# Performance work log

Hardware: AMD Instinct MI355X
Metric: run time of the kernel (lower is better)

Reference implementation:

```python
import jax, jax.numpy as jnp
import numpy as np

B, S, HID = 2, 2048, 2048
H, D = 16, 128
K = 4  # conv kernel size
EPS_L2 = 1e-6
EPS_RMS = 1e-5


def _l2norm(x, eps=EPS_L2):
  return x * jax.lax.rsqrt(jnp.sum(x * x, axis=-1, keepdims=True) + eps)


def _causal_dwconv_silu(x, w):
  # x: [B,S,C], w: [K,1,C] depthwise causal conv, then SiLU
  y = jax.lax.conv_general_dilated(
      x, w, window_strides=(1,), padding=[(w.shape[0] - 1, 0)],
      dimension_numbers=('NWC', 'WIO', 'NWC'), feature_group_count=x.shape[-1])
  return jax.nn.silu(y)


def _delta_rule(q, k, v, g, beta, scale):
  # q,k,v,g: [B,S,H,D]; beta: [B,S,H]
  qs = (q * scale).transpose(1, 0, 2, 3)  # time-major [S,B,H,D]
  ks = k.transpose(1, 0, 2, 3)
  vs = v.transpose(1, 0, 2, 3)
  gs = g.transpose(1, 0, 2, 3)
  bs = beta.transpose(1, 0, 2)  # [S,B,H]

  def step(Sst, inp):
    qt, kt, vt, gt, bt = inp  # [B,H,D], bt [B,H]
    Sst = Sst * jnp.exp(gt)[..., :, None]              # decay on k-dim: [B,H,Dk,Dv]
    err = vt - jnp.einsum('bhk,bhkv->bhv', kt, Sst)    # delta error [B,H,Dv]
    Sst = Sst + bt[..., None, None] * kt[..., :, None] * err[..., None, :]
    ot = jnp.einsum('bhk,bhkv->bhv', qt, Sst)
    return Sst, ot

  S0 = jnp.zeros((q.shape[0], q.shape[2], q.shape[3], v.shape[3]), q.dtype)
  _, outs = jax.lax.scan(step, S0, (qs, ks, vs, gs, bs))
  return outs.transpose(1, 0, 2, 3)  # [B,S,H,Dv]


def setup_inputs() -> dict:
  key = jax.random.key(0)
  ks = jax.random.split(key, 20)
  sh = 1.0 / np.sqrt(HID)
  sd = 1.0 / np.sqrt(D)
  inp = {
      'hidden_states': jax.random.normal(ks[0], (B, S, HID), jnp.float32),
      'Wq': jax.random.normal(ks[1], (HID, H * D), jnp.float32) * sh,
      'Wk': jax.random.normal(ks[2], (HID, H * D), jnp.float32) * sh,
      'Wv': jax.random.normal(ks[3], (HID, H * D), jnp.float32) * sh,
      'conv_q': jax.random.normal(ks[4], (K, 1, H * D), jnp.float32) * 0.5,
      'conv_k': jax.random.normal(ks[5], (K, 1, H * D), jnp.float32) * 0.5,
      'conv_v': jax.random.normal(ks[6], (K, 1, H * D), jnp.float32) * 0.5,
      'Wb': jax.random.normal(ks[7], (HID, H), jnp.float32) * sh,
      'Wfa': jax.random.normal(ks[8], (HID, D), jnp.float32) * sh,
      'Wfb': jax.random.normal(ks[9], (D, H * D), jnp.float32) * sd,
      'Wga': jax.random.normal(ks[10], (HID, D), jnp.float32) * sh,
      'Wgb': jax.random.normal(ks[11], (D, H * D), jnp.float32) * sd,
      'A_log': jnp.log(jax.random.uniform(ks[12], (1, 1, H, 1), jnp.float32, 1e-9, 16.0)),
      'dt_bias': jnp.ones((H * D,), jnp.float32),
      'rms_scale': jnp.ones((D,), jnp.float32),
      'Wo': jax.random.normal(ks[13], (H * D, HID), jnp.float32) * sd,
  }
  return inp


def reference(hidden_states, Wq, Wk, Wv, conv_q, conv_k, conv_v, Wb, Wfa, Wfb,
              Wga, Wgb, A_log, dt_bias, rms_scale, Wo):
  b, s, _ = hidden_states.shape
  q = _l2norm(jnp.einsum('bsd,de->bse', hidden_states, Wq).reshape(b, s, H, D))
  k = _l2norm(jnp.einsum('bsd,de->bse', hidden_states, Wk).reshape(b, s, H, D))
  v = jnp.einsum('bsd,de->bse', hidden_states, Wv).reshape(b, s, H, D)

  q = _causal_dwconv_silu(q.reshape(b, s, -1), conv_q).reshape(b, s, H, D)
  k = _causal_dwconv_silu(k.reshape(b, s, -1), conv_k).reshape(b, s, H, D)
  v = _causal_dwconv_silu(v.reshape(b, s, -1), conv_v).reshape(b, s, H, D)

  beta = jax.nn.sigmoid(jnp.einsum('bsd,dh->bsh', hidden_states, Wb))  # [B,S,H]

  # fused KDA forget gate (log-space, per k-channel)
  g_lin = jnp.einsum('bse,ef->bsf', jnp.einsum('bsd,de->bse', hidden_states, Wfa), Wfb)
  sp = jax.nn.softplus(g_lin + dt_bias).reshape(b, s, H, D)
  g_forget = -jnp.exp(A_log) * sp  # [B,S,H,D]

  attn = _delta_rule(q, k, v, g_forget, beta, scale=D ** -0.5)  # [B,S,H,D]

  # fused RMSNorm + sigmoid gate over head_dim
  gate = jnp.einsum('bse,ef->bsf', jnp.einsum('bsd,de->bse', hidden_states, Wga), Wgb).reshape(b, s, H, D)
  normed = attn * jax.lax.rsqrt(jnp.mean(attn * attn, axis=-1, keepdims=True) + EPS_RMS) * rms_scale
  out = (normed * jax.nn.sigmoid(gate)).reshape(b, s, -1)
  return jnp.einsum('bse,ed->bsd', out, Wo)
```

## Files before the change

kernel.cpp:

```cpp
#include <hip/hip_runtime.h>
#include <cstdint>

#define BB 2
#define SS 2048
#define HID_ 2048
#define HH 16
#define DD 128
#define HD 2048
#define MM 4096
#define CC 64
#define NCH 32
#define NU 1024

typedef unsigned short u16;
typedef __bf16 bf16x8 __attribute__((ext_vector_type(8)));
typedef float f32x4 __attribute__((ext_vector_type(4)));
typedef unsigned short u16x8 __attribute__((ext_vector_type(8)));

__device__ __forceinline__ u16 f2bf(float f) {
  unsigned u = __float_as_uint(f);
  u += 0x7FFFu + ((u >> 16) & 1u);
  return (u16)(u >> 16);
}
__device__ __forceinline__ float blo(unsigned u) { return __uint_as_float(u << 16); }
__device__ __forceinline__ float bhi(unsigned u) { return __uint_as_float(u & 0xffff0000u); }
__device__ __forceinline__ float sigmoidf_(float x) { return 1.0f / (1.0f + __expf(-x)); }

__device__ __forceinline__ void gll16(const void* g, void* l) {
  __builtin_amdgcn_global_load_lds((const __attribute__((address_space(1))) void*)g,
                                   (__attribute__((address_space(3))) void*)l, 16, 0, 0);
}

__global__ void cvt_bf16_kernel(const float* __restrict__ in, u16* __restrict__ out, int n) {
  int i = blockIdx.x * blockDim.x + threadIdx.x;
  if (i < n) out[i] = f2bf(in[i]);
}

__global__ __launch_bounds__(256) void transpose_bf16_kernel(
    const float* __restrict__ in, u16* __restrict__ out, int K, int N) {
  __shared__ float tile[32][33];
  int n0 = blockIdx.x * 32, k0 = blockIdx.y * 32;
  int tx = threadIdx.x, ty = threadIdx.y;
#pragma unroll
  for (int i = 0; i < 32; i += 8)
    tile[ty + i][tx] = in[(size_t)(k0 + ty + i) * N + (n0 + tx)];
  __syncthreads();
#pragma unroll
  for (int i = 0; i < 32; i += 8)
    out[(size_t)(n0 + ty + i) * K + (k0 + tx)] = f2bf(tile[tx][ty + i]);
}

__global__ __launch_bounds__(256) void gemm_bf16_kernel(
    const u16* __restrict__ A, const u16* __restrict__ Bt, float* __restrict__ C,
    int M, int N, int K) {
  __shared__ u16 As[128 * 32];
  __shared__ u16 Bs[128 * 32];
  const int tid = threadIdx.x;
  const int tileN = blockIdx.x * 128, tileM = blockIdx.y * 128;
  const int lane = tid & 63, wv = tid >> 6;
  const int wm = (wv & 1) * 64, wn = (wv >> 1) * 64;
  const int frm = lane & 15, fk = (lane >> 4) * 8;
  const int srow0 = 32 * wv + (lane >> 2);
  const int scol8 = (lane & 3) * 8;
  const u16* Ab0 = A + (size_t)(tileM + srow0) * K + scol8;
  const u16* Ab1 = A + (size_t)(tileM + srow0 + 16) * K + scol8;
  const u16* Bb0 = Bt + (size_t)(tileN + srow0) * K + scol8;
  const u16* Bb1 = Bt + (size_t)(tileN + srow0 + 16) * K + scol8;
  u16* AsL0 = &As[1024 * wv];
  u16* AsL1 = &As[1024 * wv + 512];
  u16* BsL0 = &Bs[1024 * wv];
  u16* BsL1 = &Bs[1024 * wv + 512];
  f32x4 acc[4][4];
#pragma unroll
  for (int i = 0; i < 4; ++i)
#pragma unroll
    for (int j = 0; j < 4; ++j) acc[i][j] = (f32x4)0.0f;
  for (int k0 = 0; k0 < K; k0 += 32) {
    gll16(Ab0 + k0, AsL0);
    gll16(Ab1 + k0, AsL1);
    gll16(Bb0 + k0, BsL0);
    gll16(Bb1 + k0, BsL1);
    __syncthreads();
    bf16x8 af[4], bfr[4];
#pragma unroll
    for (int t = 0; t < 4; ++t)
      af[t] = *(const bf16x8*)(&As[(wm + t * 16 + frm) * 32 + fk]);
#pragma unroll
    for (int t = 0; t < 4; ++t)
      bfr[t] = *(const bf16x8*)(&Bs[(wn + t * 16 + frm) * 32 + fk]);
#pragma unroll
    for (int mt = 0; mt < 4; ++mt)
#pragma unroll
      for (int nt = 0; nt < 4; ++nt)
        acc[mt][nt] = __builtin_amdgcn_mfma_f32_16x16x32_bf16(af[mt], bfr[nt], acc[mt][nt], 0, 0, 0);
    __syncthreads();
  }
  const int crow = (lane >> 4) * 4, ccol = lane & 15;
#pragma unroll
  for (int mt = 0; mt < 4; ++mt)
#pragma unroll
    for (int nt = 0; nt < 4; ++nt) {
      float* cp = C + (size_t)(tileM + wm + mt * 16 + crow) * N + (tileN + wn + nt * 16 + ccol);
#pragma unroll
      for (int i = 0; i < 4; ++i) cp[(size_t)i * N] = acc[mt][nt][i];
    }
}

__global__ __launch_bounds__(256) void l2norm_kernel(float* __restrict__ x) {
  int idx = blockIdx.x * 4 + (threadIdx.x >> 6);
  int lane = threadIdx.x & 63;
  float* p = x + (size_t)idx * DD;
  float2 v = *(float2*)(p + lane * 2);
  float ss = v.x * v.x + v.y * v.y;
#pragma unroll
  for (int o = 32; o > 0; o >>= 1) ss += __shfl_xor(ss, o);
  float r = rsqrtf(ss + 1e-6f);
  v.x *= r; v.y *= r;
  *(float2*)(p + lane * 2) = v;
}

__global__ void conv_silu_kernel(const float* __restrict__ x, const float* __restrict__ w,
                                 float* __restrict__ y, int n) {
  int id = blockIdx.x * blockDim.x + threadIdx.x;
  if (id >= n) return;
  int c = id & (HD - 1);
  int s = (id >> 11) & (SS - 1);
  float acc = 0.f;
#pragma unroll
  for (int t = 0; t < 4; ++t) {
    int sp = s - 3 + t;
    if (sp >= 0) acc += w[t * HD + c] * x[id + (t - 3) * HD];
  }
  y[id] = acc * sigmoidf_(acc);
}

__global__ __launch_bounds__(256) void beta_kernel(const float* __restrict__ hid,
                                                   const float* __restrict__ Wb,
                                                   float* __restrict__ beta) {
  int row = blockIdx.x;
  int tid = threadIdx.x;
  int h = tid & 15, chunk = tid >> 4;
  const float* hp = hid + (size_t)row * HID_;
  float acc = 0.f;
  int d0 = chunk * 128;
  for (int i = 0; i < 128; ++i) acc += hp[d0 + i] * Wb[(size_t)(d0 + i) * 16 + h];
  __shared__ float red[256];
  red[tid] = acc;
  __syncthreads();
  if (tid < 16) {
    float s = 0.f;
#pragma unroll
    for (int j = 0; j < 16; ++j) s += red[j * 16 + tid];
    beta[(size_t)row * 16 + tid] = 1.f / (1.f + __expf(-s));
  }
}

__global__ void kda_g_kernel(float* __restrict__ glin, const float* __restrict__ A_log,
                             const float* __restrict__ dt_bias, int n) {
  int id = blockIdx.x * blockDim.x + threadIdx.x;
  if (id >= n) return;
  int c = id & (HD - 1);
  int h = c >> 7;
  float x = glin[id] + dt_bias[c];
  float sp = (x > 20.f) ? x : log1pf(__expf(x));
  glin[id] = -__expf(A_log[h]) * sp;
}

__global__ __launch_bounds__(256) void chunk_prep(
    const float* __restrict__ q, const float* __restrict__ k, float* __restrict__ v,
    const float* __restrict__ g, const float* __restrict__ beta,
    u16* __restrict__ P, u16* __restrict__ Gt, float* __restrict__ dl,
    u16* __restrict__ Qp, u16* __restrict__ Xp) {
  __shared__ float gcl[CC * DD];
  __shared__ u16 kb[CC * DD];
  __shared__ u16 Ml[CC * CC];
  __shared__ float betal[CC];
  const int tid = threadIdx.x;
  const int chunk = blockIdx.x & 31, bh = blockIdx.x >> 5;
  const int h = bh & 15, b = bh >> 4;
  const size_t unit = (size_t)bh * NCH + chunk;
  const size_t base = ((size_t)b * SS + (size_t)chunk * CC) * HD + (size_t)h * DD;
  const float scale = 0.08838834764831845f;

  {
    int t = tid >> 2, seg = tid & 3;
    const float* kr = k + base + (size_t)t * HD + seg * 32;
    float kv[32];
#pragma unroll
    for (int i = 0; i < 8; ++i) *(f32x4*)&kv[4 * i] = *(const f32x4*)(kr + 4 * i);
    unsigned pu[16];
#pragma unroll
    for (int i = 0; i < 16; ++i)
      pu[i] = (unsigned)f2bf(kv[2 * i]) | ((unsigned)f2bf(kv[2 * i + 1]) << 16);
    uint4* dst = (uint4*)&kb[t * DD + seg * 32];
#pragma unroll
    for (int i = 0; i < 4; ++i) dst[i] = make_uint4(pu[4 * i], pu[4 * i + 1], pu[4 * i + 2], pu[4 * i + 3]);
  }
  if (tid < CC) betal[tid] = beta[((size_t)b * SS + (size_t)chunk * CC + tid) * HH + h];
  if (tid < DD) {
    int c = tid;
    float acc = 0.f;
    for (int t = 0; t < CC; ++t) {
      acc += g[base + (size_t)t * HD + c];
      gcl[t * DD + c] = acc;
    }
  }
  __syncthreads();

  {
    const int t = tid >> 2, cg = tid & 3, c0 = cg * 32;
    float kt[32], qt[32], gct[32];
#pragma unroll
    for (int i = 0; i < 8; ++i) {
      uint2 kk = ((const uint2*)&kb[t * DD + c0])[i];
      kt[4 * i + 0] = blo(kk.x); kt[4 * i + 1] = bhi(kk.x);
      kt[4 * i + 2] = blo(kk.y); kt[4 * i + 3] = bhi(kk.y);
      *(f32x4*)&gct[4 * i] = *(const f32x4*)&gcl[t * DD + c0 + 4 * i];
      *(f32x4*)&qt[4 * i] = *(const f32x4*)(q + base + (size_t)t * HD + c0 + 4 * i);
    }
#pragma unroll
    for (int i = 0; i < 32; ++i) qt[i] *= scale;
    const float bt = betal[t];
    const int jmax = ((tid >> 6) << 4) + 15;
    for (int j = 0; j <= jmax; ++j) {
      float accA = 0.f, accG = 0.f;
#pragma unroll
      for (int i = 0; i < 8; ++i) {
        uint2 kk = ((const uint2*)&kb[j * DD + c0])[i];
        f32x4 gj = *(const f32x4*)&gcl[j * DD + c0 + 4 * i];
        float e0 = __expf(gct[4 * i + 0] - gj[0]);
        float e1 = __expf(gct[4 * i + 1] - gj[1]);
        float e2 = __expf(gct[4 * i + 2] - gj[2]);
        float e3 = __expf(gct[4 * i + 3] - gj[3]);
        float p0 = blo(kk.x) * e0, p1 = bhi(kk.x) * e1;
        float p2 = blo(kk.y) * e2, p3 = bhi(kk.y) * e3;
        accA += kt[4 * i + 0] * p0 + kt[4 * i + 1] * p1 + kt[4 * i + 2] * p2 + kt[4 * i + 3] * p3;
        accG += qt[4 * i + 0] * p0 + qt[4 * i + 1] * p1 + qt[4 * i + 2] * p2 + qt[4 * i + 3] * p3;
      }
      accA += __shfl_xor(accA, 1); accA += __shfl_xor(accA, 2);
      accG += __shfl_xor(accG, 1); accG += __shfl_xor(accG, 2);
      if (cg == 0) {
        if (j <= t) {
          Gt[unit * 4096 + t * 64 + j] = f2bf(accG);
          if (j < t) Ml[t * CC + j] = f2bf(bt * accA);
        } else {
          Gt[unit * 4096 + t * 64 + j] = 0;
        }
      }
    }
    if (cg == 0)
      for (int j = jmax + 1; j < CC; ++j) Gt[unit * 4096 + t * 64 + j] = 0;
  }
  __syncthreads();

  {
    const int t = tid >> 2, seg = tid & 3;
    const size_t rb = base + (size_t)t * HD + seg * 32;
    const int e0 = t * DD + seg * 32;
    float qv[32];
#pragma unroll
    for (int i = 0; i < 8; ++i) *(f32x4*)&qv[4 * i] = *(const f32x4*)(q + rb + 4 * i);
    unsigned pu[16];
#pragma unroll
    for (int i = 0; i < 16; ++i) {
      float a = qv[2 * i] * scale * __expf(gcl[e0 + 2 * i]);
      float c2 = qv[2 * i + 1] * scale * __expf(gcl[e0 + 2 * i + 1]);
      pu[i] = (unsigned)f2bf(a) | ((unsigned)f2bf(c2) << 16);
    }
    uint4* dst = (uint4*)(Qp + unit * 8192 + t * 128 + seg * 32);
    dst[0] = make_uint4(pu[0], pu[1], pu[2], pu[3]);
    dst[1] = make_uint4(pu[4], pu[5], pu[6], pu[7]);
    ((uint4*)(Qp + unit * 8192 + t * 128 + seg * 32 + 16))[0] = make_uint4(pu[8], pu[9], pu[10], pu[11]);
    ((uint4*)(Qp + unit * 8192 + t * 128 + seg * 32 + 24))[0] = make_uint4(pu[12], pu[13], pu[14], pu[15]);
  }
  {
    const int c = tid >> 1, hf = tid & 1;
    const float glast = gcl[(CC - 1) * DD + c];
    unsigned pu[16];
#pragma unroll
    for (int i = 0; i < 16; ++i) {
      int t0 = hf * 32 + 2 * i;
      float x0 = blo((unsigned)kb[t0 * DD + c]) * __expf(glast - gcl[t0 * DD + c]);
      float x1 = blo((unsigned)kb[(t0 + 1) * DD + c]) * __expf(glast - gcl[(t0 + 1) * DD + c]);
      pu[i] = (unsigned)f2bf(x0) | ((unsigned)f2bf(x1) << 16);
    }
    uint4* dst = (uint4*)(Xp + unit * 8192 + c * 64 + hf * 32);
#pragma unroll
    for (int i = 0; i < 4; ++i)
      dst[i] = make_uint4(pu[4 * i], pu[4 * i + 1], pu[4 * i + 2], pu[4 * i + 3]);
  }
  if (tid < DD) dl[unit * DD + tid] = __expf(gcl[(CC - 1) * DD + tid]);

  {
    const int col = tid, c = col & 127;
    const bool isV = col < 128;
    float X[CC];
#pragma unroll
    for (int t = 0; t < CC; ++t) {
      float rv;
      if (isV) rv = v[base + (size_t)t * HD + c];
      else rv = blo((unsigned)kb[t * DD + c]) * __expf(gcl[t * DD + c]);
      X[t] = betal[t] * rv;
    }
#pragma unroll
    for (int i = 1; i < CC; ++i) {
      float acc = X[i];
#pragma unroll
      for (int jb = 0; jb * 8 < i; ++jb) {
        uint4 mm = *(const uint4*)&Ml[i * CC + jb * 8];
        const int j0 = jb * 8;
        if (j0 + 0 < i) acc -= blo(mm.x) * X[j0 + 0];
        if (j0 + 1 < i) acc -= bhi(mm.x) * X[j0 + 1];
        if (j0 + 2 < i) acc -= blo(mm.y) * X[j0 + 2];
        if (j0 + 3 < i) acc -= bhi(mm.y) * X[j0 + 3];
        if (j0 + 4 < i) acc -= blo(mm.z) * X[j0 + 4];
        if (j0 + 5 < i) acc -= bhi(mm.z) * X[j0 + 5];
        if (j0 + 6 < i) acc -= blo(mm.w) * X[j0 + 6];
        if (j0 + 7 < i) acc -= bhi(mm.w) * X[j0 + 7];
      }
      X[i] = acc;
    }
#pragma unroll
    for (int t = 0; t < CC; ++t) {
      if (isV) v[base + (size_t)t * HD + c] = X[t];
      else P[unit * 8192 + t * DD + c] = f2bf(X[t]);
    }
  }
}

__global__ __launch_bounds__(256) void state_pass(
    const u16* __restrict__ P, const u16* __restrict__ Xp,
    const float* __restrict__ Uvg, const float* __restrict__ dl,
    u16* __restrict__ Sst) {
  __shared__ u16 Pb[64 * 136];
  __shared__ u16 Xb[128 * 72];
  __shared__ float S[128 * 20];
  __shared__ float U[64 * 20];
  __shared__ float dll[128];
  const int tid = threadIdx.x;
  const int vs = blockIdx.x, bh = blockIdx.y;
  const int h = bh & 15, b = bh >> 4;
  for (int i = tid; i < 128 * 20; i += 256) S[i] = 0.f;
  __syncthreads();
  for (int c = 0; c < NCH; ++c) {
    const size_t unit = (size_t)bh * NCH + c;
    const size_t base = ((size_t)b * SS + (size_t)c * CC) * HD + (size_t)h * DD + vs * 16;
#pragma unroll
    for (int r = 0; r < 4; ++r) {
      int e = r * 256 + tid;
      int t = e >> 4, kp = (e & 15) * 8;
      *(uint4*)&Pb[t * 136 + kp] = ((const uint4*)(P + unit * 8192))[e];
      int kk = e >> 3, tp = (e & 7) * 8;
      *(uint4*)&Xb[kk * 72 + tp] = ((const uint4*)(Xp + unit * 8192))[e];
    }
    {
      int t = tid >> 2, cg = tid & 3;
      *(f32x4*)&U[t * 20 + cg * 4] = *(const f32x4*)(Uvg + base + (size_t)t * HD + cg * 4);
    }
    if (tid < 128) dll[tid] = dl[unit * DD + tid];
    {
      int v2 = tid >> 4, kq = tid & 15;
      unsigned pu[4];
#pragma unroll
      for (int j = 0; j < 4; ++j) {
        float a = S[(kq * 8 + 2 * j) * 20 + v2];
        float bb = S[(kq * 8 + 2 * j + 1) * 20 + v2];
        pu[j] = (unsigned)f2bf(a) | ((unsigned)f2bf(bb) << 16);
      }
      *(uint4*)(Sst + unit * 16384 + (size_t)(vs * 16 + v2) * 128 + kq * 8) =
          make_uint4(pu[0], pu[1], pu[2], pu[3]);
    }
    __syncthreads();
    {
      const int t = tid >> 2, cg = tid & 3;
      f32x4 u = *(f32x4*)&U[t * 20 + cg * 4];
      f32x4 acc = (f32x4)0.f;
      for (int kk = 0; kk < 128; kk += 4) {
        uint2 pk = *(const uint2*)&Pb[t * 136 + kk];
        f32x4 s0 = *(const f32x4*)&S[(kk + 0) * 20 + cg * 4];
        f32x4 s1 = *(const f32x4*)&S[(kk + 1) * 20 + cg * 4];
        f32x4 s2 = *(const f32x4*)&S[(kk + 2) * 20 + cg * 4];
        f32x4 s3 = *(const f32x4*)&S[(kk + 3) * 20 + cg * 4];
        acc += blo(pk.x) * s0;
        acc += bhi(pk.x) * s1;
        acc += blo(pk.y) * s2;
        acc += bhi(pk.y) * s3;
      }
      u -= acc;
      *(f32x4*)&U[t * 20 + cg * 4] = u;
    }
    __syncthreads();
    {
      const int kk = tid >> 1, cg2 = tid & 1;
      f32x4 sa = *(f32x4*)&S[kk * 20 + cg2 * 8];
      f32x4 sb = *(f32x4*)&S[kk * 20 + cg2 * 8 + 4];
      float dk = dll[kk];
      sa *= dk; sb *= dk;
      for (int t4 = 0; t4 < 64; t4 += 4) {
        uint2 xv = *(const uint2*)&Xb[kk * 72 + t4];
        float x0 = blo(xv.x), x1 = bhi(xv.x), x2 = blo(xv.y), x3 = bhi(xv.y);
        f32x4 u0a = *(const f32x4*)&U[(t4 + 0) * 20 + cg2 * 8];
        f32x4 u0b = *(const f32x4*)&U[(t4 + 0) * 20 + cg2 * 8 + 4];
        f32x4 u1a = *(const f32x4*)&U[(t4 + 1) * 20 + cg2 * 8];
        f32x4 u1b = *(const f32x4*)&U[(t4 + 1) * 20 + cg2 * 8 + 4];
        f32x4 u2a = *(const f32x4*)&U[(t4 + 2) * 20 + cg2 * 8];
        f32x4 u2b = *(const f32x4*)&U[(t4 + 2) * 20 + cg2 * 8 + 4];
        f32x4 u3a = *(const f32x4*)&U[(t4 + 3) * 20 + cg2 * 8];
        f32x4 u3b = *(const f32x4*)&U[(t4 + 3) * 20 + cg2 * 8 + 4];
        sa += x0 * u0a; sb += x0 * u0b;
        sa += x1 * u1a; sb += x1 * u1b;
        sa += x2 * u2a; sb += x2 * u2b;
        sa += x3 * u3a; sb += x3 * u3b;
      }
      *(f32x4*)&S[kk * 20 + cg2 * 8] = sa;
      *(f32x4*)&S[kk * 20 + cg2 * 8 + 4] = sb;
    }
    __syncthreads();
  }
}

__global__ __launch_bounds__(256) void out_pass(
    const u16* __restrict__ P, const u16* __restrict__ Qp,
    const u16* __restrict__ G, const u16* __restrict__ Sst,
    const float* __restrict__ Uvg, float* __restrict__ attn) {
  __shared__ u16 Sb[128 * 136];
  __shared__ u16 Pb[64 * 136];
  __shared__ u16 Qb[64 * 136];
  __shared__ u16 Gb[64 * 72];
  __shared__ u16 Ub[128 * 72];
  const int tid = threadIdx.x;
  const int unit = blockIdx.x;
  const int bh = unit >> 5, c = unit & 31;
  const int h = bh & 15, b = bh >> 4;
  const size_t base = ((size_t)b * SS + (size_t)c * CC) * HD + (size_t)h * DD;
#pragma unroll
  for (int r = 0; r < 8; ++r) {
    int e = r * 256 + tid;
    int v = e >> 4, kp = (e & 15) * 8;
    *(uint4*)&Sb[v * 136 + kp] = ((const uint4*)(Sst + (size_t)unit * 16384))[e];
  }
#pragma unroll
  for (int r = 0; r < 4; ++r) {
    int e = r * 256 + tid;
    int t = e >> 4, kp = (e & 15) * 8;
    *(uint4*)&Pb[t * 136 + kp] = ((const uint4*)(P + (size_t)unit * 8192))[e];
    *(uint4*)&Qb[t * 136 + kp] = ((const uint4*)(Qp + (size_t)unit * 8192))[e];
  }
#pragma unroll
  for (int r = 0; r < 2; ++r) {
    int e = r * 256 + tid;
    int t = e >> 3, jp = (e & 7) * 8;
    *(uint4*)&Gb[t * 72 + jp] = ((const uint4*)(G + (size_t)unit * 4096))[e];
  }
  __syncthreads();
  const int w = tid >> 6, lane = tid & 63;
  const int frm = lane & 15, fk = (lane >> 4) * 8;
  const int crow = (lane >> 4) * 4, ccol = lane & 15;
  bf16x8 Pf[4], Qf[4], Gf[2];
#pragma unroll
  for (int kb2 = 0; kb2 < 4; ++kb2) {
    Pf[kb2] = *(const bf16x8*)&Pb[(w * 16 + frm) * 136 + kb2 * 32 + fk];
    Qf[kb2] = *(const bf16x8*)&Qb[(w * 16 + frm) * 136 + kb2 * 32 + fk];
  }
#pragma unroll
  for (int kb2 = 0; kb2 < 2; ++kb2)
    Gf[kb2] = *(const bf16x8*)&Gb[(w * 16 + frm) * 72 + kb2 * 32 + fk];
  f32x4 aps[8], ao[8];
#pragma unroll
  for (int nt = 0; nt < 8; ++nt) { aps[nt] = (f32x4)0.f; ao[nt] = (f32x4)0.f; }
#pragma unroll
  for (int nt = 0; nt < 8; ++nt)
#pragma unroll
    for (int kb2 = 0; kb2 < 4; ++kb2) {
      bf16x8 sf = *(const bf16x8*)&Sb[(nt * 16 + frm) * 136 + kb2 * 32 + fk];
      aps[nt] = __builtin_amdgcn_mfma_f32_16x16x32_bf16(Pf[kb2], sf, aps[nt], 0, 0, 0);
      ao[nt] = __builtin_amdgcn_mfma_f32_16x16x32_bf16(Qf[kb2], sf, ao[nt], 0, 0, 0);
    }
#pragma unroll
  for (int nt = 0; nt < 8; ++nt) {
    float un[4];
#pragma unroll
    for (int i = 0; i < 4; ++i) {
      float uv = Uvg[base + (size_t)(w * 16 + crow + i) * HD + nt * 16 + ccol];
      un[i] = uv - aps[nt][i];
    }
    uint2 pk = make_uint2((unsigned)f2bf(un[0]) | ((unsigned)f2bf(un[1]) << 16),
                          (unsigned)f2bf(un[2]) | ((unsigned)f2bf(un[3]) << 16));
    *(uint2*)&Ub[(nt * 16 + ccol) * 72 + w * 16 + crow] = pk;
  }
  __syncthreads();
#pragma unroll
  for (int nt = 0; nt < 8; ++nt)
#pragma unroll
    for (int kb2 = 0; kb2 < 2; ++kb2) {
      bf16x8 uf = *(const bf16x8*)&Ub[(nt * 16 + frm) * 72 + kb2 * 32 + fk];
      ao[nt] = __builtin_amdgcn_mfma_f32_16x16x32_bf16(Gf[kb2], uf, ao[nt], 0, 0, 0);
    }
#pragma unroll
  for (int nt = 0; nt < 8; ++nt)
#pragma unroll
    for (int i = 0; i < 4; ++i)
      attn[base + (size_t)(w * 16 + crow + i) * HD + nt * 16 + ccol] = ao[nt][i];
}

__global__ __launch_bounds__(256) void gate_rms_kernel(
    const float* __restrict__ attn, const float* __restrict__ gate,
    const float* __restrict__ rms_scale, u16* __restrict__ preout) {
  int idx = blockIdx.x * 4 + (threadIdx.x >> 6);
  int lane = threadIdx.x & 63;
  const float* ap = attn + (size_t)idx * DD;
  const float* gp = gate + (size_t)idx * DD;
  float2 a = *(const float2*)(ap + lane * 2);
  float ss = a.x * a.x + a.y * a.y;
#pragma unroll
  for (int o = 32; o > 0; o >>= 1) ss += __shfl_xor(ss, o);
  float r = rsqrtf(ss * (1.0f / 128.0f) + 1e-5f);
  float2 gg = *(const float2*)(gp + lane * 2);
  int d = lane * 2;
  float o0 = a.x * r * rms_scale[d] * sigmoidf_(gg.x);
  float o1 = a.y * r * rms_scale[d + 1] * sigmoidf_(gg.y);
  preout[(size_t)idx * DD + d] = f2bf(o0);
  preout[(size_t)idx * DD + d + 1] = f2bf(o1);
}

extern "C" void kernel_launch(void* const* d_in, const int* in_sizes, int n_in,
                              void* d_out, int out_size, void* d_ws, size_t ws_size,
                              hipStream_t stream) {
  const float* hid = (const float*)d_in[0];
  const float* Wq = (const float*)d_in[1];
  const float* Wk = (const float*)d_in[2];
  const float* Wv = (const float*)d_in[3];
  const float* conv_q = (const float*)d_in[4];
  const float* conv_k = (const float*)d_in[5];
  const float* conv_v = (const float*)d_in[6];
  const float* Wb = (const float*)d_in[7];
  const float* Wfa = (const float*)d_in[8];
  const float* Wfb = (const float*)d_in[9];
  const float* Wga = (const float*)d_in[10];
  const float* Wgb = (const float*)d_in[11];
  const float* A_log = (const float*)d_in[12];
  const float* dt_bias = (const float*)d_in[13];
  const float* rms_scale = (const float*)d_in[14];
  const float* Wo = (const float*)d_in[15];
  float* out = (float*)d_out;
  (void)in_sizes; (void)n_in; (void)out_size; (void)ws_size;

  char* w = (char*)d_ws;
  size_t off = 0;
  auto alloc = [&](size_t bytes) -> void* {
    void* p = w + off;
    off += (bytes + 255) & ~(size_t)255;
    return p;
  };
  u16* hidb = (u16*)alloc((size_t)MM * HID_ * 2);
  u16* WqT  = (u16*)alloc((size_t)HD * HID_ * 2);
  u16* WkT  = (u16*)alloc((size_t)HD * HID_ * 2);
  u16* WvT  = (u16*)alloc((size_t)HD * HID_ * 2);
  u16* WoT  = (u16*)alloc((size_t)HID_ * HD * 2);
  u16* WfaT = (u16*)alloc((size_t)DD * HID_ * 2);
  u16* WgaT = (u16*)alloc((size_t)DD * HID_ * 2);
  u16* WfbT = (u16*)alloc((size_t)HD * DD * 2);
  u16* WgbT = (u16*)alloc((size_t)HD * DD * 2);
  float* X1 = (float*)alloc((size_t)MM * HD * 4);
  float* X2 = (float*)alloc((size_t)MM * HD * 4);
  float* X3 = (float*)alloc((size_t)MM * HD * 4);
  float* T  = (float*)alloc((size_t)MM * HD * 4);
  float* beta = (float*)alloc((size_t)MM * HH * 4);
  float* fa = (float*)alloc((size_t)MM * DD * 4);
  float* ga = (float*)alloc((size_t)MM * DD * 4);
  u16* fab = (u16*)alloc((size_t)MM * DD * 2);
  u16* gab = (u16*)alloc((size_t)MM * DD * 2);
  u16* Xp  = (u16*)alloc((size_t)NU * 8192 * 2);
  u16* Qp  = WkT;
  u16* Sst = (u16*)X3;

  dim3 tb(32, 8);
  const int n_full = MM * HD;

  cvt_bf16_kernel<<<(n_full + 255) / 256, 256, 0, stream>>>(hid, hidb, n_full);
  transpose_bf16_kernel<<<dim3(HD / 32, HID_ / 32), tb, 0, stream>>>(Wq, WqT, HID_, HD);
  transpose_bf16_kernel<<<dim3(HD / 32, HID_ / 32), tb, 0, stream>>>(Wk, WkT, HID_, HD);
  transpose_bf16_kernel<<<dim3(HD / 32, HID_ / 32), tb, 0, stream>>>(Wv, WvT, HID_, HD);
  transpose_bf16_kernel<<<dim3(HID_ / 32, HD / 32), tb, 0, stream>>>(Wo, WoT, HD, HID_);
  transpose_bf16_kernel<<<dim3(DD / 32, HID_ / 32), tb, 0, stream>>>(Wfa, WfaT, HID_, DD);
  transpose_bf16_kernel<<<dim3(DD / 32, HID_ / 32), tb, 0, stream>>>(Wga, WgaT, HID_, DD);
  transpose_bf16_kernel<<<dim3(HD / 32, DD / 32), tb, 0, stream>>>(Wfb, WfbT, DD, HD);
  transpose_bf16_kernel<<<dim3(HD / 32, DD / 32), tb, 0, stream>>>(Wgb, WgbT, DD, HD);

  gemm_bf16_kernel<<<dim3(HD / 128, MM / 128), 256, 0, stream>>>(hidb, WqT, X1, MM, HD, HID_);
  gemm_bf16_kernel<<<dim3(HD / 128, MM / 128), 256, 0, stream>>>(hidb, WkT, X2, MM, HD, HID_);
  gemm_bf16_kernel<<<dim3(HD / 128, MM / 128), 256, 0, stream>>>(hidb, WvT, X3, MM, HD, HID_);
  gemm_bf16_kernel<<<dim3(DD / 128, MM / 128), 256, 0, stream>>>(hidb, WfaT, fa, MM, DD, HID_);
  gemm_bf16_kernel<<<dim3(DD / 128, MM / 128), 256, 0, stream>>>(hidb, WgaT, ga, MM, DD, HID_);
  beta_kernel<<<MM, 256, 0, stream>>>(hid, Wb, beta);

  l2norm_kernel<<<MM * HH / 4, 256, 0, stream>>>(X1);
  l2norm_kernel<<<MM * HH / 4, 256, 0, stream>>>(X2);

  conv_silu_kernel<<<(n_full + 255) / 256, 256, 0, stream>>>(X1, conv_q, T, n_full);
  conv_silu_kernel<<<(n_full + 255) / 256, 256, 0, stream>>>(X2, conv_k, X1, n_full);
  conv_silu_kernel<<<(n_full + 255) / 256, 256, 0, stream>>>(X3, conv_v, X2, n_full);

  cvt_bf16_kernel<<<(MM * DD + 255) / 256, 256, 0, stream>>>(fa, fab, MM * DD);
  gemm_bf16_kernel<<<dim3(HD / 128, MM / 128), 256, 0, stream>>>(fab, WfbT, X3, MM, HD, DD);
  kda_g_kernel<<<(n_full + 255) / 256, 256, 0, stream>>>(X3, A_log, dt_bias, n_full);

  chunk_prep<<<NU, 256, 0, stream>>>(T, X1, X2, X3, beta, hidb, WqT, fa, Qp, Xp);
  state_pass<<<dim3(8, 32), 256, 0, stream>>>(hidb, Xp, X2, fa, Sst);
  out_pass<<<NU, 256, 0, stream>>>(hidb, Qp, WqT, Sst, X2, out);

  cvt_bf16_kernel<<<(MM * DD + 255) / 256, 256, 0, stream>>>(ga, gab, MM * DD);
  gemm_bf16_kernel<<<dim3(HD / 128, MM / 128), 256, 0, stream>>>(gab, WgbT, T, MM, HD, DD);

  gate_rms_kernel<<<MM * HH / 4, 256, 0, stream>>>(out, T, rms_scale, hidb);

  gemm_bf16_kernel<<<dim3(HID_ / 128, MM / 128), 256, 0, stream>>>(hidb, WoT, out, MM, HID_, HD);
}
```

Baseline: 1.248 ms.

## Split chunk prep into MFMA-based intra-chunk gram kernel and separate triangular solve

Splits the chunk preparation kernel in two. The new first kernel computes the intra-chunk decayed K·K and Q·K gram matrices blockwise: diagonal 16x16 blocks in scalar fp32, off-diagonal blocks with bf16 MFMA on rebased decay factors. It writes M and beta-weighted decayed keys to scratch held in the output buffer. A second kernel loads these and performs the forward triangular solve, which spreads register pressure and lets the gram work use matrix cores. The cost is extra global round-trips for the scratch data, an additional launch, and possible precision loss from the rebased bf16 decay products.

```diff
diff --git a/kernel.cpp b/kernel.cpp
--- a/kernel.cpp
+++ b/kernel.cpp
@@ -29,6 +29,26 @@
 __device__ __forceinline__ void gll16(const void* g, void* l) {
   __builtin_amdgcn_global_load_lds((const __attribute__((address_space(1))) void*)g,
                                    (__attribute__((address_space(3))) void*)l, 16, 0, 0);
+}
+
+typedef union { unsigned q[4]; bf16x8 b; } fragu;
+
+__device__ __forceinline__ bf16x8 decay_row8(const u16* kr, const float* gr, const float* ar, int off) {
+  uint4 k8 = *(const uint4*)(kr + off);
+  f32x4 g0 = *(const f32x4*)(gr + off);
+  f32x4 g1 = *(const f32x4*)(gr + off + 4);
+  f32x4 a0 = *(const f32x4*)(ar + off);
+  f32x4 a1 = *(const f32x4*)(ar + off + 4);
+  fragu r;
+  r.q[0] = (unsigned)f2bf(blo(k8.x) * __expf(g0[0] - a0[0])) |
+           ((unsigned)f2bf(bhi(k8.x) * __expf(g0[1] - a0[1])) << 16);
+  r.q[1] = (unsigned)f2bf(blo(k8.y) * __expf(g0[2] - a0[2])) |
+           ((unsigned)f2bf(bhi(k8.y) * __expf(g0[3] - a0[3])) << 16);
+  r.q[2] = (unsigned)f2bf(blo(k8.z) * __expf(g1[0] - a1[0])) |
+           ((unsigned)f2bf(bhi(k8.z) * __expf(g1[1] - a1[1])) << 16);
+  r.q[3] = (unsigned)f2bf(blo(k8.w) * __expf(g1[2] - a1[2])) |
+           ((unsigned)f2bf(bhi(k8.w) * __expf(g1[3] - a1[3])) << 16);
+  return r.b;
 }
 
 __global__ void cvt_bf16_kernel(const float* __restrict__ in, u16* __restrict__ out, int n) {
@@ -166,13 +186,187 @@
   glin[id] = -__expf(A_log[h]) * sp;
 }
 
-__global__ __launch_bounds__(256) void chunk_prep(
-    const float* __restrict__ q, const float* __restrict__ k, float* __restrict__ v,
+__global__ __launch_bounds__(256) void chunk_prepA(
+    const float* __restrict__ q, const float* __restrict__ k,
     const float* __restrict__ g, const float* __restrict__ beta,
-    u16* __restrict__ P, u16* __restrict__ Gt, float* __restrict__ dl,
-    u16* __restrict__ Qp, u16* __restrict__ Xp) {
-  __shared__ float gcl[CC * DD];
-  __shared__ u16 kb[CC * DD];
+    u16* __restrict__ Gt, u16* __restrict__ Mg, u16* __restrict__ Wg,
+    float* __restrict__ dl, u16* __restrict__ Qp, u16* __restrict__ Xp) {
+  __shared__ float gcl[CC * 132];
+  __shared__ u16 kb[CC * 136];
+  __shared__ u16 qd[16 * 128];
+  __shared__ u16 Gli[16 * 64];
+  __shared__ u16 MlI[16 * 64];
+  const int tid = threadIdx.x;
+  const int chunk = blockIdx.x & 31, bh = blockIdx.x >> 5;
+  const int h = bh & 15, b = bh >> 4;
+  const size_t unit = (size_t)bh * NCH + chunk;
+  const size_t base = ((size_t)b * SS + (size_t)chunk * CC) * HD + (size_t)h * DD;
+  const float scale = 0.08838834764831845f;
+  const int w = tid >> 6, lane = tid & 63;
+  const int frm = lane & 15, fk = (lane >> 4) * 8;
+  const int crow = (lane >> 4) * 4, ccol = lane & 15;
+
+  {
+    int t = tid >> 2, seg = tid & 3;
+    const float* kr = k + base + (size_t)t * HD + seg * 32;
+    float kv[32];
+#pragma unroll
+    for (int i = 0; i < 8; ++i) *(f32x4*)&kv[4 * i] = *(const f32x4*)(kr + 4 * i);
+    unsigned pu[16];
+#pragma unroll
+    for (int i = 0; i < 16; ++i)
+      pu[i] = (unsigned)f2bf(kv[2 * i]) | ((unsigned)f2bf(kv[2 * i + 1]) << 16);
+    uint4* dst = (uint4*)&kb[t * 136 + seg * 32];
+#pragma unroll
+    for (int i = 0; i < 4; ++i) dst[i] = make_uint4(pu[4 * i], pu[4 * i + 1], pu[4 * i + 2], pu[4 * i + 3]);
+  }
+  if (tid < CC) gcl[tid * 132 + 128] = beta[((size_t)b * SS + (size_t)chunk * CC + tid) * HH + h];
+  if (tid < DD) {
+    float acc = 0.f;
+    for (int t = 0; t < CC; ++t) {
+      acc += g[base + (size_t)t * HD + tid];
+      gcl[t * 132 + tid] = acc;
+    }
+  }
+  __syncthreads();
+
+#pragma unroll 1
+  for (int I = 0; I < 4; ++I) {
+    const int aI = 16 * I;
+    for (int e = tid; e < 512; e += 256) ((unsigned*)Gli)[e] = 0;
+    {
+      int tl = tid >> 4, c0 = (tid & 15) * 8;
+      const float* qr = q + base + (size_t)(aI + tl) * HD + c0;
+      f32x4 q0 = *(const f32x4*)qr;
+      f32x4 q1 = *(const f32x4*)(qr + 4);
+      uint4 o;
+      o.x = (unsigned)f2bf(q0[0] * scale) | ((unsigned)f2bf(q0[1] * scale) << 16);
+      o.y = (unsigned)f2bf(q0[2] * scale) | ((unsigned)f2bf(q0[3] * scale) << 16);
+      o.z = (unsigned)f2bf(q1[0] * scale) | ((unsigned)f2bf(q1[1] * scale) << 16);
+      o.w = (unsigned)f2bf(q1[2] * scale) | ((unsigned)f2bf(q1[3] * scale) << 16);
+      *(uint4*)&qd[tl * 128 + c0] = o;
+    }
+    __syncthreads();
+    {
+      const int tl = tid >> 4, jl = tid & 15;
+      const int rt = aI + tl, rj = aI + jl;
+      float accA = 0.f, accG = 0.f;
+#pragma unroll
+      for (int c0 = 0; c0 < 128; c0 += 8) {
+        f32x4 gt0 = *(const f32x4*)&gcl[rt * 132 + c0];
+        f32x4 gt1 = *(const f32x4*)&gcl[rt * 132 + c0 + 4];
+        f32x4 gj0 = *(const f32x4*)&gcl[rj * 132 + c0];
+        f32x4 gj1 = *(const f32x4*)&gcl[rj * 132 + c0 + 4];
+        uint4 kt4 = *(const uint4*)&kb[rt * 136 + c0];
+        uint4 kj4 = *(const uint4*)&kb[rj * 136 + c0];
+        uint4 qt4 = *(const uint4*)&qd[tl * 128 + c0];
+        float e, p;
+        e = __expf(gt0[0] - gj0[0]); p = blo(kj4.x) * e; accA += blo(kt4.x) * p; accG += blo(qt4.x) * p;
+        e = __expf(gt0[1] - gj0[1]); p = bhi(kj4.x) * e; accA += bhi(kt4.x) * p; accG += bhi(qt4.x) * p;
+        e = __expf(gt0[2] - gj0[2]); p = blo(kj4.y) * e; accA += blo(kt4.y) * p; accG += blo(qt4.y) * p;
+        e = __expf(gt0[3] - gj0[3]); p = bhi(kj4.y) * e; accA += bhi(kt4.y) * p; accG += bhi(qt4.y) * p;
+        e = __expf(gt1[0] - gj1[0]); p = blo(kj4.z) * e; accA += blo(kt4.z) * p; accG += blo(qt4.z) * p;
+        e = __expf(gt1[1] - gj1[1]); p = bhi(kj4.z) * e; accA += bhi(kt4.z) * p; accG += bhi(qt4.z) * p;
+        e = __expf(gt1[2] - gj1[2]); p = blo(kj4.w) * e; accA += blo(kt4.w) * p; accG += blo(qt4.w) * p;
+        e = __expf(gt1[3] - gj1[3]); p = bhi(kj4.w) * e; accA += bhi(kt4.w) * p; accG += bhi(qt4.w) * p;
+      }
+      if (jl <= tl) Gli[tl * 64 + aI + jl] = f2bf(accG);
+      if (jl < tl) MlI[tl * 64 + aI + jl] = f2bf(gcl[rt * 132 + 128] * accA);
+    }
+    if (w < 2) {
+      const int rt = aI + frm;
+      bf16x8 af[4];
+#pragma unroll
+      for (int kb2 = 0; kb2 < 4; ++kb2) {
+        int off = kb2 * 32 + fk;
+        if (w == 0)
+          af[kb2] = decay_row8(&kb[rt * 136], &gcl[rt * 132], &gcl[aI * 132], off);
+        else
+          af[kb2] = decay_row8(&qd[frm * 128], &gcl[rt * 132], &gcl[aI * 132], off);
+      }
+      for (int J = 0; J < I; ++J) {
+        const int rj = 16 * J + frm;
+        f32x4 acc = (f32x4)0.f;
+#pragma unroll
+        for (int kb2 = 0; kb2 < 4; ++kb2) {
+          int off = kb2 * 32 + fk;
+          bf16x8 bf = decay_row8(&kb[rj * 136], &gcl[aI * 132], &gcl[rj * 132], off);
+          acc = __builtin_amdgcn_mfma_f32_16x16x32_bf16(af[kb2], bf, acc, 0, 0, 0);
+        }
+        if (w == 0) {
+#pragma unroll
+          for (int i = 0; i < 4; ++i) {
+            float bt = gcl[(aI + crow + i) * 132 + 128];
+            MlI[(crow + i) * 64 + 16 * J + ccol] = f2bf(bt * acc[i]);
+          }
+        } else {
+#pragma unroll
+          for (int i = 0; i < 4; ++i)
+            Gli[(crow + i) * 64 + 16 * J + ccol] = f2bf(acc[i]);
+        }
+      }
+    }
+    __syncthreads();
+    if (tid < 128) {
+      int t = tid >> 3, j0 = (tid & 7) * 8;
+      *(uint4*)(Gt + unit * 4096 + (size_t)(aI + t) * 64 + j0) = *(const uint4*)&Gli[t * 64 + j0];
+    } else {
+      int t2 = (tid - 128) >> 3, j0 = ((tid - 128) & 7) * 8;
+      *(uint4*)(Mg + unit * 4096 + (size_t)(aI + t2) * 64 + j0) = *(const uint4*)&MlI[t2 * 64 + j0];
+    }
+    {
+      int tl = tid >> 4, c0 = (tid & 15) * 8;
+      const int rt = aI + tl;
+      uint4 q8 = *(const uint4*)&qd[tl * 128 + c0];
+      f32x4 g0 = *(const f32x4*)&gcl[rt * 132 + c0];
+      f32x4 g1 = *(const f32x4*)&gcl[rt * 132 + c0 + 4];
+      uint4 o;
+      o.x = (unsigned)f2bf(blo(q8.x) * __expf(g0[0])) | ((unsigned)f2bf(bhi(q8.x) * __expf(g0[1])) << 16);
+      o.y = (unsigned)f2bf(blo(q8.y) * __expf(g0[2])) | ((unsigned)f2bf(bhi(q8.y) * __expf(g0[3])) << 16);
+      o.z = (unsigned)f2bf(blo(q8.z) * __expf(g1[0])) | ((unsigned)f2bf(bhi(q8.z) * __expf(g1[1])) << 16);
+      o.w = (unsigned)f2bf(blo(q8.w) * __expf(g1[2])) | ((unsigned)f2bf(bhi(q8.w) * __expf(g1[3])) << 16);
+      *(uint4*)(Qp + unit * 8192 + (size_t)rt * 128 + c0) = o;
+    }
+    __syncthreads();
+  }
+
+#pragma unroll
+  for (int r = 0; r < 4; ++r) {
+    int c = (tid >> 3) + r * 32;
+    int t8 = (tid & 7) * 8;
+    float gl = gcl[63 * 132 + c];
+    unsigned pu[4];
+#pragma unroll
+    for (int i = 0; i < 4; ++i) {
+      int t0 = t8 + 2 * i;
+      float x0 = blo((unsigned)kb[t0 * 136 + c]) * __expf(gl - gcl[t0 * 132 + c]);
+      float x1 = blo((unsigned)kb[(t0 + 1) * 136 + c]) * __expf(gl - gcl[(t0 + 1) * 132 + c]);
+      pu[i] = (unsigned)f2bf(x0) | ((unsigned)f2bf(x1) << 16);
+    }
+    *(uint4*)(Xp + unit * 8192 + (size_t)c * 64 + t8) = make_uint4(pu[0], pu[1], pu[2], pu[3]);
+  }
+  if (tid < DD) dl[unit * DD + tid] = __expf(gcl[63 * 132 + tid]);
+  {
+    int t = tid >> 2, c0 = (tid & 3) * 32;
+    float bt = gcl[t * 132 + 128];
+#pragma unroll
+    for (int s4 = 0; s4 < 4; ++s4) {
+      uint4 k8 = *(const uint4*)&kb[t * 136 + c0 + s4 * 8];
+      f32x4 g0 = *(const f32x4*)&gcl[t * 132 + c0 + s4 * 8];
+      f32x4 g1 = *(const f32x4*)&gcl[t * 132 + c0 + s4 * 8 + 4];
+      uint4 o;
+      o.x = (unsigned)f2bf(bt * blo(k8.x) * __expf(g0[0])) | ((unsigned)f2bf(bt * bhi(k8.x) * __expf(g0[1])) << 16);
+      o.y = (unsigned)f2bf(bt * blo(k8.y) * __expf(g0[2])) | ((unsigned)f2bf(bt * bhi(k8.y) * __expf(g0[3])) << 16);
+      o.z = (unsigned)f2bf(bt * blo(k8.z) * __expf(g1[0])) | ((unsigned)f2bf(bt * bhi(k8.z) * __expf(g1[1])) << 16);
+      o.w = (unsigned)f2bf(bt * blo(k8.w) * __expf(g1[2])) | ((unsigned)f2bf(bt * bhi(k8.w) * __expf(g1[3])) << 16);
+      *(uint4*)(Wg + unit * 8192 + (size_t)t * 128 + c0 + s4 * 8) = o;
+    }
+  }
+}
+
+__global__ __launch_bounds__(256) void solve_kernel(
+    const u16* __restrict__ Mg, const u16* __restrict__ Wg,
+    float* __restrict__ v, const float* __restrict__ beta, u16* __restrict__ P) {
   __shared__ u16 Ml[CC * CC];
   __shared__ float betal[CC];
   const int tid = threadIdx.x;
@@ -180,151 +374,40 @@
   const int h = bh & 15, b = bh >> 4;
   const size_t unit = (size_t)bh * NCH + chunk;
   const size_t base = ((size_t)b * SS + (size_t)chunk * CC) * HD + (size_t)h * DD;
-  const float scale = 0.08838834764831845f;
-
-  {
-    int t = tid >> 2, seg = tid & 3;
-    const float* kr = k + base + (size_t)t * HD + seg * 32;
-    float kv[32];
-#pragma unroll
-    for (int i = 0; i < 8; ++i) *(f32x4*)&kv[4 * i] = *(const f32x4*)(kr + 4 * i);
-    unsigned pu[16];
-#pragma unroll
-    for (int i = 0; i < 16; ++i)
-      pu[i] = (unsigned)f2bf(kv[2 * i]) | ((unsigned)f2bf(kv[2 * i + 1]) << 16);
-    uint4* dst = (uint4*)&kb[t * DD + seg * 32];
-#pragma unroll
-    for (int i = 0; i < 4; ++i) dst[i] = make_uint4(pu[4 * i], pu[4 * i + 1], pu[4 * i + 2], pu[4 * i + 3]);
-  }
+  ((uint4*)Ml)[tid] = ((const uint4*)(Mg + unit * 4096))[tid];
+  ((uint4*)Ml)[tid + 256] = ((const uint4*)(Mg + unit * 4096))[tid + 256];
   if (tid < CC) betal[tid] = beta[((size_t)b * SS + (size_t)chunk * CC + tid) * HH + h];
-  if (tid < DD) {
-    int c = tid;
-    float acc = 0.f;
-    for (int t = 0; t < CC; ++t) {
-      acc += g[base + (size_t)t * HD + c];
-      gcl[t * DD + c] = acc;
-    }
-  }
   __syncthreads();
-
-  {
-    const int t = tid >> 2, cg = tid & 3, c0 = cg * 32;
-    float kt[32], qt[32], gct[32];
-#pragma unroll
-    for (int i = 0; i < 8; ++i) {
-      uint2 kk = ((const uint2*)&kb[t * DD + c0])[i];
-      kt[4 * i + 0] = blo(kk.x); kt[4 * i + 1] = bhi(kk.x);
-      kt[4 * i + 2] = blo(kk.y); kt[4 * i + 3] = bhi(kk.y);
-      *(f32x4*)&gct[4 * i] = *(const f32x4*)&gcl[t * DD + c0 + 4 * i];
-      *(f32x4*)&qt[4 * i] = *(const f32x4*)(q + base + (size_t)t * HD + c0 + 4 * i);
-    }
-#pragma unroll
-    for (int i = 0; i < 32; ++i) qt[i] *= scale;
-    const float bt = betal[t];
-    const int jmax = ((tid >> 6) << 4) + 15;
-    for (int j = 0; j <= jmax; ++j) {
-      float accA = 0.f, accG = 0.f;
-#pragma unroll
-      for (int i = 0; i < 8; ++i) {
-        uint2 kk = ((const uint2*)&kb[j * DD + c0])[i];
-        f32x4 gj = *(const f32x4*)&gcl[j * DD + c0 + 4 * i];
-        float e0 = __expf(gct[4 * i + 0] - gj[0]);
-        float e1 = __expf(gct[4 * i + 1] - gj[1]);
-        float e2 = __expf(gct[4 * i + 2] - gj[2]);
-        float e3 = __expf(gct[4 * i + 3] - gj[3]);
-        float p0 = blo(kk.x) * e0, p1 = bhi(kk.x) * e1;
-        float p2 = blo(kk.y) * e2, p3 = bhi(kk.y) * e3;
-        accA += kt[4 * i + 0] * p0 + kt[4 * i + 1] * p1 + kt[4 * i + 2] * p2 + kt[4 * i + 3] * p3;
-        accG += qt[4 * i + 0] * p0 + qt[4 * i + 1] * p1 + qt[4 * i + 2] * p2 + qt[4 * i + 3] * p3;
-      }
-      accA += __shfl_xor(accA, 1); accA += __shfl_xor(accA, 2);
-      accG += __shfl_xor(accG, 1); accG += __shfl_xor(accG, 2);
-      if (cg == 0) {
-        if (j <= t) {
-          Gt[unit * 4096 + t * 64 + j] = f2bf(accG);
-          if (j < t) Ml[t * CC + j] = f2bf(bt * accA);
-        } else {
-          Gt[unit * 4096 + t * 64 + j] = 0;
-        }
-      }
-    }
-    if (cg == 0)
-      for (int j = jmax + 1; j < CC; ++j) Gt[unit * 4096 + t * 64 + j] = 0;
-  }
-  __syncthreads();
-
-  {
-    const int t = tid >> 2, seg = tid & 3;
-    const size_t rb = base + (size_t)t * HD + seg * 32;
-    const int e0 = t * DD + seg * 32;
-    float qv[32];
-#pragma unroll
-    for (int i = 0; i < 8; ++i) *(f32x4*)&qv[4 * i] = *(const f32x4*)(q + rb + 4 * i);
-    unsigned pu[16];
-#pragma unroll
-    for (int i = 0; i < 16; ++i) {
-      float a = qv[2 * i] * scale * __expf(gcl[e0 + 2 * i]);
-      float c2 = qv[2 * i + 1] * scale * __expf(gcl[e0 + 2 * i + 1]);
-      pu[i] = (unsigned)f2bf(a) | ((unsigned)f2bf(c2) << 16);
-    }
-    uint4* dst = (uint4*)(Qp + unit * 8192 + t * 128 + seg * 32);
-    dst[0] = make_uint4(pu[0], pu[1], pu[2], pu[3]);
-    dst[1] = make_uint4(pu[4], pu[5], pu[6], pu[7]);
-    ((uint4*)(Qp + unit * 8192 + t * 128 + seg * 32 + 16))[0] = make_uint4(pu[8], pu[9], pu[10], pu[11]);
-    ((uint4*)(Qp + unit * 8192 + t * 128 + seg * 32 + 24))[0] = make_uint4(pu[12], pu[13], pu[14], pu[15]);
-  }
-  {
-    const int c = tid >> 1, hf = tid & 1;
-    const float glast = gcl[(CC - 1) * DD + c];
-    unsigned pu[16];
-#pragma unroll
-    for (int i = 0; i < 16; ++i) {
-      int t0 = hf * 32 + 2 * i;
-      float x0 = blo((unsigned)kb[t0 * DD + c]) * __expf(glast - gcl[t0 * DD + c]);
-      float x1 = blo((unsigned)kb[(t0 + 1) * DD + c]) * __expf(glast - gcl[(t0 + 1) * DD + c]);
-      pu[i] = (unsigned)f2bf(x0) | ((unsigned)f2bf(x1) << 16);
-    }
-    uint4* dst = (uint4*)(Xp + unit * 8192 + c * 64 + hf * 32);
-#pragma unroll
-    for (int i = 0; i < 4; ++i)
-      dst[i] = make_uint4(pu[4 * i], pu[4 * i + 1], pu[4 * i + 2], pu[4 * i + 3]);
-  }
-  if (tid < DD) dl[unit * DD + tid] = __expf(gcl[(CC - 1) * DD + tid]);
-
-  {
-    const int col = tid, c = col & 127;
-    const bool isV = col < 128;
-    float X[CC];
-#pragma unroll
-    for (int t = 0; t < CC; ++t) {
-      float rv;
-      if (isV) rv = v[base + (size_t)t * HD + c];
-      else rv = blo((unsigned)kb[t * DD + c]) * __expf(gcl[t * DD + c]);
-      X[t] = betal[t] * rv;
-    }
-#pragma unroll
-    for (int i = 1; i < CC; ++i) {
-      float acc = X[i];
-#pragma unroll
-      for (int jb = 0; jb * 8 < i; ++jb) {
-        uint4 mm = *(const uint4*)&Ml[i * CC + jb * 8];
-        const int j0 = jb * 8;
-        if (j0 + 0 < i) acc -= blo(mm.x) * X[j0 + 0];
-        if (j0 + 1 < i) acc -= bhi(mm.x) * X[j0 + 1];
-        if (j0 + 2 < i) acc -= blo(mm.y) * X[j0 + 2];
-        if (j0 + 3 < i) acc -= bhi(mm.y) * X[j0 + 3];
-        if (j0 + 4 < i) acc -= blo(mm.z) * X[j0 + 4];
-        if (j0 + 5 < i) acc -= bhi(mm.z) * X[j0 + 5];
-        if (j0 + 6 < i) acc -= blo(mm.w) * X[j0 + 6];
-        if (j0 + 7 < i) acc -= bhi(mm.w) * X[j0 + 7];
-      }
-      X[i] = acc;
-    }
-#pragma unroll
-    for (int t = 0; t < CC; ++t) {
-      if (isV) v[base + (size_t)t * HD + c] = X[t];
-      else P[unit * 8192 + t * DD + c] = f2bf(X[t]);
-    }
+  const int c = tid & 127;
+  const bool isV = tid < 128;
+  float X[CC];
+#pragma unroll
+  for (int t = 0; t < CC; ++t) {
+    if (isV) X[t] = betal[t] * v[base + (size_t)t * HD + c];
+    else X[t] = blo((unsigned)Wg[unit * 8192 + t * 128 + c]);
+  }
+#pragma unroll
+  for (int i = 1; i < CC; ++i) {
+    float acc = X[i];
+#pragma unroll
+    for (int jb = 0; jb * 8 < i; ++jb) {
+      uint4 mm = *(const uint4*)&Ml[i * CC + jb * 8];
+      const int j0 = jb * 8;
+      if (j0 + 0 < i) acc -= blo(mm.x) * X[j0 + 0];
+      if (j0 + 1 < i) acc -= bhi(mm.x) * X[j0 + 1];
+      if (j0 + 2 < i) acc -= blo(mm.y) * X[j0 + 2];
+      if (j0 + 3 < i) acc -= bhi(mm.y) * X[j0 + 3];
+      if (j0 + 4 < i) acc -= blo(mm.z) * X[j0 + 4];
+      if (j0 + 5 < i) acc -= bhi(mm.z) * X[j0 + 5];
+      if (j0 + 6 < i) acc -= blo(mm.w) * X[j0 + 6];
+      if (j0 + 7 < i) acc -= bhi(mm.w) * X[j0 + 7];
+    }
+    X[i] = acc;
+  }
+#pragma unroll
+  for (int t = 0; t < CC; ++t) {
+    if (isV) v[base + (size_t)t * HD + c] = X[t];
+    else P[unit * 8192 + t * 128 + c] = f2bf(X[t]);
   }
 }
 
@@ -573,6 +656,8 @@
   u16* Xp  = (u16*)alloc((size_t)NU * 8192 * 2);
   u16* Qp  = WkT;
   u16* Sst = (u16*)X3;
+  u16* Mg  = (u16*)d_out;
+  u16* Wg  = (u16*)d_out + (size_t)NU * 4096;
 
   dim3 tb(32, 8);
   const int n_full = MM * HD;
@@ -605,7 +690,8 @@
   gemm_bf16_kernel<<<dim3(HD / 128, MM / 128), 256, 0, stream>>>(fab, WfbT, X3, MM, HD, DD);
   kda_g_kernel<<<(n_full + 255) / 256, 256, 0, stream>>>(X3, A_log, dt_bias, n_full);
 
-  chunk_prep<<<NU, 256, 0, stream>>>(T, X1, X2, X3, beta, hidb, WqT, fa, Qp, Xp);
+  chunk_prepA<<<NU, 256, 0, stream>>>(T, X1, X3, beta, WqT, Mg, Wg, fa, Qp, Xp);
+  solve_kernel<<<NU, 256, 0, stream>>>(Mg, Wg, X2, beta, hidb);
   state_pass<<<dim3(8, 32), 256, 0, stream>>>(hidb, Xp, X2, fa, Sst);
   out_pass<<<NU, 256, 0, stream>>>(hidb, Qp, WqT, Sst, X2, out);
 
```

After: 1.277 ms. 2.3% more time.
